# Kernel optimization log

Measured on AMD Instinct MI355X. Metric: run time of the kernel, lower is better.

## Reference

```python
import jax, jax.numpy as jnp
import numpy as np

N = 100000          # nodes
E = 3200000         # edges
C_IN = 64
HIDDEN = 64
NUM_CLASSES = 10
NUM_GRAPHS = 256
EPS = 1e-5


def _graph_conv(x, src, dst, w_rel, w_root, b):
    # PyG GraphConv(aggr='mean'): out_i = W_rel * mean_{j->i} x_j + W_root * x_i + b
    msg_sum = jax.ops.segment_sum(x[src], dst, num_segments=N)            # [N, C]
    cnt = jax.ops.segment_sum(jnp.ones((src.shape[0], 1), x.dtype), dst,
                              num_segments=N)                             # [N, 1]
    agg = msg_sum / jnp.maximum(cnt, 1.0)
    return agg @ w_rel + x @ w_root + b


def _batch_norm(x, gamma, beta):
    # PyG BatchNorm in training mode: batch stats over the node dimension
    mean = jnp.mean(x, axis=0)
    var = jnp.var(x, axis=0)
    return (x - mean) * jax.lax.rsqrt(var + EPS) * gamma + beta


def setup_inputs() -> dict:
    key = jax.random.key(0)
    ks = jax.random.split(key, 20)
    x = jax.random.normal(ks[0], (N, C_IN), dtype=jnp.float32)
    edge_index = jax.random.randint(ks[1], (2, E), 0, N, dtype=jnp.int32)
    batch = jnp.sort(jax.random.randint(ks[2], (N,), 0, NUM_GRAPHS, dtype=jnp.int32))

    def lin(k, fan_in, fan_out):
        s = 1.0 / np.sqrt(fan_in)
        return jax.random.uniform(k, (fan_in, fan_out), jnp.float32, -s, s)

    dims = [(C_IN, 16), (16, 32), (32, 32), (32, HIDDEN)]
    params = {}
    ki = 3
    for i, (ci, co) in enumerate(dims, start=1):
        params[f"w_rel{i}"] = lin(ks[ki], ci, co); ki += 1
        params[f"w_root{i}"] = lin(ks[ki], ci, co); ki += 1
        params[f"b{i}"] = jnp.zeros((co,), jnp.float32)
        params[f"g{i}"] = jnp.ones((co,), jnp.float32)
        params[f"be{i}"] = jnp.zeros((co,), jnp.float32)
    params["w_lin1"] = lin(ks[ki], HIDDEN, HIDDEN); ki += 1
    params["b_lin1"] = jnp.zeros((HIDDEN,), jnp.float32)
    params["w_lin2"] = lin(ks[ki], HIDDEN, NUM_CLASSES); ki += 1
    params["b_lin2"] = jnp.zeros((NUM_CLASSES,), jnp.float32)

    return {"x": x, "edge_index": edge_index, "batch": batch, **params}


def reference(x, edge_index, batch,
              w_rel1, w_root1, b1, g1, be1,
              w_rel2, w_root2, b2, g2, be2,
              w_rel3, w_root3, b3, g3, be3,
              w_rel4, w_root4, b4, g4, be4,
              w_lin1, b_lin1, w_lin2, b_lin2):
    src, dst = edge_index[0], edge_index[1]
    h = jax.nn.elu(_batch_norm(_graph_conv(x, src, dst, w_rel1, w_root1, b1), g1, be1))
    h = jax.nn.elu(_batch_norm(_graph_conv(h, src, dst, w_rel2, w_root2, b2), g2, be2))
    h = jax.nn.elu(_batch_norm(_graph_conv(h, src, dst, w_rel3, w_root3, b3), g3, be3))
    h = jax.nn.elu(_batch_norm(_graph_conv(h, src, dst, w_rel4, w_root4, b4), g4, be4))
    # global mean pool over graphs
    pooled = jax.ops.segment_sum(h, batch, num_segments=NUM_GRAPHS)
    cnt = jax.ops.segment_sum(jnp.ones((N, 1), h.dtype), batch, num_segments=NUM_GRAPHS)
    pooled = pooled / jnp.maximum(cnt, 1.0)
    z = jax.nn.relu(pooled @ w_lin1 + b_lin1)
    # dropout omitted (deterministic / eval mode)
    logits = z @ w_lin2 + b_lin2
    return jax.nn.log_softmax(logits, axis=-1)
```

## Files before the change

### kernel.cpp

```cpp
#include <hip/hip_runtime.h>
#include <hip/hip_bf16.h>
#include <math.h>

#define NGRAPHS 256
#define BSHIFT 8
#define NBUCK 512
#define NSORT 256
#define SBLK 256
#define SMASK 0x00FFFFFFu

__device__ __forceinline__ float bf2f(unsigned short u) {
    return __uint_as_float((unsigned)u << 16);
}
__device__ __forceinline__ unsigned short f2bf(float f) {
    unsigned u = __float_as_uint(f);
    unsigned r = (u + 0x7FFFu + ((u >> 16) & 1u)) >> 16;
    return (unsigned short)r;
}

__global__ __launch_bounds__(256) void k_bhist(const int* __restrict__ dst, int* __restrict__ hmat, int E) {
    __shared__ int hist[NBUCK];
    for (int i = threadIdx.x; i < NBUCK; i += 256) hist[i] = 0;
    __syncthreads();
    int chunk = (E + NSORT - 1) / NSORT;
    int lo = blockIdx.x * chunk;
    int hi = lo + chunk; if (hi > E) hi = E;
    for (int i = lo + threadIdx.x; i < hi; i += 256) {
        int d = __builtin_nontemporal_load(dst + i);
        atomicAdd(&hist[d >> BSHIFT], 1);
    }
    __syncthreads();
    for (int i = threadIdx.x; i < NBUCK; i += 256)
        hmat[(size_t)blockIdx.x * NBUCK + i] = hist[i];
}

__global__ __launch_bounds__(256) void k_cscan(int* __restrict__ hmat, int* __restrict__ btot) {
    int col = blockIdx.x * 256 + threadIdx.x;
    int run = 0;
#pragma unroll 4
    for (int r = 0; r < NSORT; r++) {
        int v = hmat[(size_t)r * NBUCK + col];
        hmat[(size_t)r * NBUCK + col] = run;
        run += v;
    }
    btot[col] = run;
}

__global__ __launch_bounds__(512) void k_bscan(const int* __restrict__ btot, int* __restrict__ bstart) {
    __shared__ int s[512];
    int tid = threadIdx.x;
    int v = btot[tid];
    s[tid] = v;
    __syncthreads();
    for (int off = 1; off < 512; off <<= 1) {
        int t = (tid >= off) ? s[tid - off] : 0;
        __syncthreads();
        s[tid] += t;
        __syncthreads();
    }
    bstart[tid] = s[tid] - v;
    if (tid == 511) bstart[NBUCK] = s[511];
}

__global__ __launch_bounds__(256) void k_bscatter(const int* __restrict__ src, const int* __restrict__ dst,
                                                  const int* __restrict__ hmat, const int* __restrict__ bstart,
                                                  unsigned* __restrict__ ebuf, int E) {
    __shared__ int cur[NBUCK];
    for (int i = threadIdx.x; i < NBUCK; i += 256)
        cur[i] = bstart[i] + hmat[(size_t)blockIdx.x * NBUCK + i];
    __syncthreads();
    int chunk = (E + NSORT - 1) / NSORT;
    int lo = blockIdx.x * chunk;
    int hi = lo + chunk; if (hi > E) hi = E;
    for (int i = lo + threadIdx.x; i < hi; i += 256) {
        int d = __builtin_nontemporal_load(dst + i);
        int s = __builtin_nontemporal_load(src + i);
        int p = atomicAdd(&cur[d >> BSHIFT], 1);
        ebuf[p] = (unsigned)s | ((unsigned)(d & 255) << 24);
    }
}

__global__ __launch_bounds__(256) void k_sort2(const unsigned* __restrict__ ebuf, const int* __restrict__ bstart,
                                               int* __restrict__ csr, int* __restrict__ row_start, int N) {
    __shared__ int hist[256];
    __shared__ int sc[256];
    __shared__ int scur[256];
    int b = blockIdx.x;
    int e0 = bstart[b], e1 = bstart[b + 1];
    hist[threadIdx.x] = 0;
    __syncthreads();
    for (int i = e0 + threadIdx.x; i < e1; i += 256)
        atomicAdd(&hist[__builtin_nontemporal_load(ebuf + i) >> 24], 1);
    __syncthreads();
    sc[threadIdx.x] = hist[threadIdx.x];
    __syncthreads();
    for (int off = 1; off < 256; off <<= 1) {
        int t = (threadIdx.x >= off) ? sc[threadIdx.x - off] : 0;
        __syncthreads();
        sc[threadIdx.x] += t;
        __syncthreads();
    }
    {
        int inc = sc[threadIdx.x];
        int ex = inc - hist[threadIdx.x];
        scur[threadIdx.x] = e0 + ex;
        int node = (b << BSHIFT) + threadIdx.x;
        if (node < N) row_start[node] = e0 + ex;
        if (node == N - 1) row_start[N] = e0 + inc;
    }
    __syncthreads();
    for (int i = e0 + threadIdx.x; i < e1; i += 256) {
        unsigned w = __builtin_nontemporal_load(ebuf + i);
        int p = atomicAdd(&scur[w >> 24], 1);
        csr[p] = (int)(w & SMASK);
    }
}

template <int CI, int CO, bool HAS_REL, bool HAS_ROOT, bool ADD_AGG, bool HAS_BIAS, bool IN_BF16, bool OUT_BF16>
__global__ __launch_bounds__(256) void k_lin(const void* __restrict__ hroot_v, const float* __restrict__ hrel,
                                             const float* __restrict__ w_rel, const float* __restrict__ w_root,
                                             const float* __restrict__ bias, const float* __restrict__ aggadd,
                                             float* __restrict__ out, unsigned short* __restrict__ outb, int N) {
    constexpr int QPR = CO / 4;
    __shared__ float s_rel[HAS_REL ? CI * CO : 1];
    __shared__ float s_root[HAS_ROOT ? CI * CO : 1];
    __shared__ float s_b[HAS_BIAS ? CO : 4];
    if (HAS_REL)
        for (int i = threadIdx.x; i < CI * CO; i += 256) s_rel[i] = w_rel[i];
    if (HAS_ROOT)
        for (int i = threadIdx.x; i < CI * CO; i += 256) s_root[i] = w_root[i];
    if (HAS_BIAS && threadIdx.x < CO) s_b[threadIdx.x] = bias[threadIdx.x];
    __syncthreads();

    int t = blockIdx.x * 256 + threadIdx.x;
    int n = t / QPR;
    int c0 = (t % QPR) * 4;
    if (n >= N) return;

    float rr[HAS_ROOT ? CI : 1];
    if (HAS_ROOT) {
        if (IN_BF16) {
            const ushort4* hp = (const ushort4*)((const unsigned short*)hroot_v + (size_t)n * CI);
#pragma unroll
            for (int i = 0; i < CI / 4; i++) {
                ushort4 v = hp[i];
                rr[4 * i + 0] = bf2f(v.x); rr[4 * i + 1] = bf2f(v.y);
                rr[4 * i + 2] = bf2f(v.z); rr[4 * i + 3] = bf2f(v.w);
            }
        } else {
            const float4* hp = (const float4*)((const float*)hroot_v + (size_t)n * CI);
#pragma unroll
            for (int i = 0; i < CI / 4; i++) {
                float4 v = hp[i];
                rr[4 * i + 0] = v.x; rr[4 * i + 1] = v.y; rr[4 * i + 2] = v.z; rr[4 * i + 3] = v.w;
            }
        }
    }
    float ar[HAS_REL ? CI : 1];
    if (HAS_REL) {
        const float4* mp = (const float4*)(hrel + (size_t)n * CI);
#pragma unroll
        for (int i = 0; i < CI / 4; i++) {
            float4 v = mp[i];
            ar[4 * i + 0] = v.x; ar[4 * i + 1] = v.y; ar[4 * i + 2] = v.z; ar[4 * i + 3] = v.w;
        }
    }

    float4 acc;
    if (HAS_BIAS) acc = *(const float4*)&s_b[c0];
    else { acc.x = 0.f; acc.y = 0.f; acc.z = 0.f; acc.w = 0.f; }
    if (ADD_AGG) {
        float4 v = *(const float4*)(aggadd + (size_t)n * CO + c0);
        acc.x += v.x; acc.y += v.y; acc.z += v.z; acc.w += v.w;
    }

#pragma unroll
    for (int ci = 0; ci < CI; ci++) {
        if (HAS_REL) {
            float a = ar[ci];
            float4 w = *(const float4*)&s_rel[ci * CO + c0];
            acc.x += a * w.x; acc.y += a * w.y; acc.z += a * w.z; acc.w += a * w.w;
        }
        if (HAS_ROOT) {
            float hv = rr[ci];
            float4 w = *(const float4*)&s_root[ci * CO + c0];
            acc.x += hv * w.x; acc.y += hv * w.y; acc.z += hv * w.z; acc.w += hv * w.w;
        }
    }
    if (OUT_BF16) {
        ushort4 o;
        o.x = f2bf(acc.x); o.y = f2bf(acc.y); o.z = f2bf(acc.z); o.w = f2bf(acc.w);
        *(ushort4*)(outb + (size_t)n * CO + c0) = o;
    } else {
        *(float4*)(out + (size_t)n * CO + c0) = acc;
    }
}

template <int C>
__global__ __launch_bounds__(256) void k_gather(const unsigned short* __restrict__ h,
                                                const int* __restrict__ row_start,
                                                const int* __restrict__ csr, float* __restrict__ agg, int N) {
    constexpr int LPR = C / 4;
    constexpr int EPP = 64 / LPR;
    int lane = threadIdx.x & 63;
    int wid = blockIdx.x * 4 + (threadIdx.x >> 6);
    if (wid >= N) return;
    int r0 = row_start[wid];
    int deg = row_start[wid + 1] - r0;
    int es = lane / LPR;
    int cq = (lane % LPR) * 4;
    float ax = 0.f, ay = 0.f, az = 0.f, aw = 0.f;
    for (int j0 = 0; j0 < deg; j0 += 4 * EPP) {
        int s[4]; bool p[4];
#pragma unroll
        for (int u = 0; u < 4; u++) {
            int j = j0 + u * EPP + es;
            p[u] = j < deg;
            s[u] = __builtin_nontemporal_load(&csr[r0 + (p[u] ? j : 0)]);
        }
#pragma unroll
        for (int u = 0; u < 4; u++) {
            ushort4 v = *(const ushort4*)(h + (size_t)s[u] * C + cq);
            if (p[u]) {
                ax += bf2f(v.x); ay += bf2f(v.y); az += bf2f(v.z); aw += bf2f(v.w);
            }
        }
    }
#pragma unroll
    for (int off = LPR; off < 64; off <<= 1) {
        ax += __shfl_xor(ax, off, 64);
        ay += __shfl_xor(ay, off, 64);
        az += __shfl_xor(az, off, 64);
        aw += __shfl_xor(aw, off, 64);
    }
    if (lane < LPR) {
        float rec = 1.0f / (float)(deg > 0 ? deg : 1);
        float4 o; o.x = ax * rec; o.y = ay * rec; o.z = az * rec; o.w = aw * rec;
        *(float4*)(agg + (size_t)wid * C + cq) = o;
    }
}

template <int CO>
__global__ __launch_bounds__(256) void k_stats(const float* __restrict__ h, float* __restrict__ partials, int N) {
    constexpr int QPR = CO / 4;
    int total = N * QPR;
    float s0 = 0, s1 = 0, s2 = 0, s3 = 0, q0 = 0, q1 = 0, q2 = 0, q3 = 0;
    int idx = blockIdx.x * 256 + threadIdx.x;
    for (int i = idx; i < total; i += SBLK * 256) {
        float4 v = ((const float4*)h)[i];
        s0 += v.x; q0 += v.x * v.x;
        s1 += v.y; q1 += v.y * v.y;
        s2 += v.z; q2 += v.z * v.z;
        s3 += v.w; q3 += v.w * v.w;
    }
#pragma unroll
    for (int off = QPR; off < 64; off <<= 1) {
        s0 += __shfl_xor(s0, off, 64); q0 += __shfl_xor(q0, off, 64);
        s1 += __shfl_xor(s1, off, 64); q1 += __shfl_xor(q1, off, 64);
        s2 += __shfl_xor(s2, off, 64); q2 += __shfl_xor(q2, off, 64);
        s3 += __shfl_xor(s3, off, 64); q3 += __shfl_xor(q3, off, 64);
    }
    __shared__ float part[4][2 * CO];
    int lane = threadIdx.x & 63;
    int w = threadIdx.x >> 6;
    if (lane < QPR) {
        int cq = lane * 4;
        part[w][cq + 0] = s0; part[w][CO + cq + 0] = q0;
        part[w][cq + 1] = s1; part[w][CO + cq + 1] = q1;
        part[w][cq + 2] = s2; part[w][CO + cq + 2] = q2;
        part[w][cq + 3] = s3; part[w][CO + cq + 3] = q3;
    }
    __syncthreads();
    if (threadIdx.x < 2 * CO) {
        float v = part[0][threadIdx.x] + part[1][threadIdx.x] + part[2][threadIdx.x] + part[3][threadIdx.x];
        partials[blockIdx.x * (2 * CO) + threadIdx.x] = v;
    }
}

__global__ __launch_bounds__(128) void k_sfinal(const float* __restrict__ partials, const float* __restrict__ g,
                                                const float* __restrict__ be, float* __restrict__ stats,
                                                int CO, float invN) {
    __shared__ float red[128];
    int c = threadIdx.x;
    float s = 0.f;
    if (c < 2 * CO) {
        for (int b = 0; b < SBLK; b++) s += partials[b * 2 * CO + c];
    }
    red[c] = s;
    __syncthreads();
    if (c < CO) {
        float mean = red[c] * invN;
        float var = red[CO + c] * invN - mean * mean;
        float sc = g[c] * rsqrtf(var + 1e-5f);
        stats[128 + c] = sc;
        stats[192 + c] = be[c] - mean * sc;
    }
}

template <int CO>
__global__ __launch_bounds__(256) void k_bn_elu(const float* __restrict__ h, const float* __restrict__ stats,
                                                unsigned short* __restrict__ hb, int N) {
    __shared__ float sc[CO], sh[CO];
    if (threadIdx.x < CO) {
        sc[threadIdx.x] = stats[128 + threadIdx.x];
        sh[threadIdx.x] = stats[192 + threadIdx.x];
    }
    __syncthreads();
    int total = N * (CO / 4);
    int i = blockIdx.x * 256 + threadIdx.x;
    if (i >= total) return;
    float4 v = ((const float4*)h)[i];
    int cq = (i % (CO / 4)) * 4;
    v.x = v.x * sc[cq + 0] + sh[cq + 0];
    v.y = v.y * sc[cq + 1] + sh[cq + 1];
    v.z = v.z * sc[cq + 2] + sh[cq + 2];
    v.w = v.w * sc[cq + 3] + sh[cq + 3];
    v.x = v.x > 0.f ? v.x : expm1f(v.x);
    v.y = v.y > 0.f ? v.y : expm1f(v.y);
    v.z = v.z > 0.f ? v.z : expm1f(v.z);
    v.w = v.w > 0.f ? v.w : expm1f(v.w);
    ushort4 o;
    o.x = f2bf(v.x); o.y = f2bf(v.y); o.z = f2bf(v.z); o.w = f2bf(v.w);
    ((ushort4*)hb)[i] = o;
}

__global__ __launch_bounds__(256) void k_pool(const unsigned short* __restrict__ hb, const int* __restrict__ batch,
                                              float* __restrict__ pooled, float* __restrict__ cntg, int N) {
    int lane = threadIdx.x & 63;
    int wid = blockIdx.x * 4 + (threadIdx.x >> 6);
    int n0 = wid * 64;
    if (n0 >= N) return;
    int nmax = N - n0; if (nmax > 64) nmax = 64;
    int cur = batch[n0];
    float acc = 0.f;
    int run = 0;
    for (int k = 0; k < nmax; k++) {
        int g = batch[n0 + k];
        if (g != cur) {
            atomicAdd(&pooled[(size_t)cur * 64 + lane], acc);
            if (lane == 0) atomicAdd(&cntg[cur], (float)run);
            cur = g; acc = 0.f; run = 0;
        }
        acc += bf2f(hb[(size_t)(n0 + k) * 64 + lane]);
        run++;
    }
    atomicAdd(&pooled[(size_t)cur * 64 + lane], acc);
    if (lane == 0) atomicAdd(&cntg[cur], (float)run);
}

__global__ __launch_bounds__(256) void k_head(const float* __restrict__ pooled, const float* __restrict__ cntg,
                                              const float* __restrict__ w1, const float* __restrict__ b1,
                                              const float* __restrict__ w2, const float* __restrict__ b2,
                                              float* __restrict__ out) {
    int g = threadIdx.x;
    float rec = 1.0f / fmaxf(cntg[g], 1.0f);
    float p[64];
    {
        const float4* pp = (const float4*)(pooled + (size_t)g * 64);
#pragma unroll
        for (int i = 0; i < 16; i++) {
            float4 v = pp[i];
            p[4 * i + 0] = v.x * rec; p[4 * i + 1] = v.y * rec;
            p[4 * i + 2] = v.z * rec; p[4 * i + 3] = v.w * rec;
        }
    }
    float lg[10];
#pragma unroll
    for (int t = 0; t < 10; t++) lg[t] = b2[t];
#pragma unroll 1
    for (int j = 0; j < 64; j++) {
        float a = b1[j];
#pragma unroll
        for (int k = 0; k < 64; k++) a += p[k] * w1[k * 64 + j];
        a = fmaxf(a, 0.f);
#pragma unroll
        for (int t = 0; t < 10; t++) lg[t] += a * w2[j * 10 + t];
    }
    float m = -1e30f;
#pragma unroll
    for (int t = 0; t < 10; t++) m = fmaxf(m, lg[t]);
    float s = 0.f;
#pragma unroll
    for (int t = 0; t < 10; t++) s += expf(lg[t] - m);
    float lse = m + logf(s);
#pragma unroll
    for (int t = 0; t < 10; t++) out[(size_t)g * 10 + t] = lg[t] - lse;
}

extern "C" void kernel_launch(void* const* d_in, const int* in_sizes, int n_in,
                              void* d_out, int out_size, void* d_ws, size_t ws_size,
                              hipStream_t stream) {
    const float* x = (const float*)d_in[0];
    const int* ei = (const int*)d_in[1];
    const int* batch = (const int*)d_in[2];
    const int N = in_sizes[0] / 64;
    const int E = in_sizes[1] / 2;
    const int* src = ei;
    const int* dst = ei + E;

    const float* w_rel1 = (const float*)d_in[3];
    const float* w_root1 = (const float*)d_in[4];
    const float* b1 = (const float*)d_in[5];
    const float* g1 = (const float*)d_in[6];
    const float* be1 = (const float*)d_in[7];
    const float* w_rel2 = (const float*)d_in[8];
    const float* w_root2 = (const float*)d_in[9];
    const float* b2 = (const float*)d_in[10];
    const float* g2 = (const float*)d_in[11];
    const float* be2 = (const float*)d_in[12];
    const float* w_rel3 = (const float*)d_in[13];
    const float* w_root3 = (const float*)d_in[14];
    const float* b3 = (const float*)d_in[15];
    const float* g3 = (const float*)d_in[16];
    const float* be3 = (const float*)d_in[17];
    const float* w_rel4 = (const float*)d_in[18];
    const float* w_root4 = (const float*)d_in[19];
    const float* b4 = (const float*)d_in[20];
    const float* g4 = (const float*)d_in[21];
    const float* be4 = (const float*)d_in[22];
    const float* w_lin1 = (const float*)d_in[23];
    const float* b_lin1 = (const float*)d_in[24];
    const float* w_lin2 = (const float*)d_in[25];
    const float* b_lin2 = (const float*)d_in[26];

    char* ws = (char*)d_ws;
    size_t off = 0;
    auto alloc = [&](size_t bytes) { size_t o = off; off += (bytes + 255) & ~(size_t)255; return o; };
    int* hmat = (int*)(ws + alloc((size_t)NSORT * NBUCK * 4));
    int* btot = (int*)(ws + alloc((size_t)NBUCK * 4));
    int* bstart = (int*)(ws + alloc((size_t)(NBUCK + 1) * 4));
    unsigned* ebuf = (unsigned*)(ws + alloc((size_t)E * 4));
    int* csr = (int*)(ws + alloc((size_t)E * 4));
    int* row_start = (int*)(ws + alloc((size_t)(N + 1) * 4));
    float* agg = (float*)(ws + alloc((size_t)N * 32 * 4));
    unsigned short* y1b = (unsigned short*)(ws + alloc((size_t)N * 16 * 2));
    unsigned short* hb = (unsigned short*)(ws + alloc((size_t)N * 64 * 2));
    float* bufA = (float*)(ws + alloc((size_t)N * 64 * 4));
    float* stats = (float*)(ws + alloc(4 * 256 * 4));
    float* partials = (float*)(ws + alloc((size_t)SBLK * 128 * 4));
    float* pooled = (float*)(ws + alloc((size_t)(NGRAPHS * 64 + NGRAPHS) * 4));
    float* cntg = pooled + NGRAPHS * 64;

    hipMemsetAsync(pooled, 0, (size_t)(NGRAPHS * 64 + NGRAPHS) * 4, stream);

    const float invN = 1.0f / (float)N;
    const int gbl = (N + 3) / 4;
    auto lgrid = [&](int qpr) { return (N * qpr + 255) / 256; };

    k_bhist<<<NSORT, 256, 0, stream>>>(dst, hmat, E);
    k_cscan<<<NBUCK / 256, 256, 0, stream>>>(hmat, btot);
    k_bscan<<<1, 512, 0, stream>>>(btot, bstart);
    k_bscatter<<<NSORT, 256, 0, stream>>>(src, dst, hmat, bstart, ebuf, E);
    k_sort2<<<NBUCK, 256, 0, stream>>>(ebuf, bstart, csr, row_start, N);

    k_lin<64, 16, true, false, false, false, false, true><<<lgrid(4), 256, 0, stream>>>(
        nullptr, x, w_rel1, nullptr, nullptr, nullptr, nullptr, y1b, N);
    k_gather<16><<<gbl, 256, 0, stream>>>(y1b, row_start, csr, agg, N);
    k_lin<64, 16, false, true, true, true, false, false><<<lgrid(4), 256, 0, stream>>>(
        x, nullptr, nullptr, w_root1, b1, agg, bufA, nullptr, N);
    k_stats<16><<<SBLK, 256, 0, stream>>>(bufA, partials, N);
    k_sfinal<<<1, 128, 0, stream>>>(partials, g1, be1, stats + 0, 16, invN);
    k_bn_elu<16><<<(N * 4 + 255) / 256, 256, 0, stream>>>(bufA, stats + 0, hb, N);

    k_gather<16><<<gbl, 256, 0, stream>>>(hb, row_start, csr, agg, N);
    k_lin<16, 32, true, true, false, true, true, false><<<lgrid(8), 256, 0, stream>>>(
        hb, agg, w_rel2, w_root2, b2, nullptr, bufA, nullptr, N);
    k_stats<32><<<SBLK, 256, 0, stream>>>(bufA, partials, N);
    k_sfinal<<<1, 128, 0, stream>>>(partials, g2, be2, stats + 256, 32, invN);
    k_bn_elu<32><<<(N * 8 + 255) / 256, 256, 0, stream>>>(bufA, stats + 256, hb, N);

    k_gather<32><<<gbl, 256, 0, stream>>>(hb, row_start, csr, agg, N);
    k_lin<32, 32, true, true, false, true, true, false><<<lgrid(8), 256, 0, stream>>>(
        hb, agg, w_rel3, w_root3, b3, nullptr, bufA, nullptr, N);
    k_stats<32><<<SBLK, 256, 0, stream>>>(bufA, partials, N);
    k_sfinal<<<1, 128, 0, stream>>>(partials, g3, be3, stats + 512, 32, invN);
    k_bn_elu<32><<<(N * 8 + 255) / 256, 256, 0, stream>>>(bufA, stats + 512, hb, N);

    k_gather<32><<<gbl, 256, 0, stream>>>(hb, row_start, csr, agg, N);
    k_lin<32, 64, true, true, false, true, true, false><<<lgrid(16), 256, 0, stream>>>(
        hb, agg, w_rel4, w_root4, b4, nullptr, bufA, nullptr, N);
    k_stats<64><<<SBLK, 256, 0, stream>>>(bufA, partials, N);
    k_sfinal<<<1, 128, 0, stream>>>(partials, g4, be4, stats + 768, 64, invN);
    k_bn_elu<64><<<(N * 16 + 255) / 256, 256, 0, stream>>>(bufA, stats + 768, hb, N);

    int waves = (N + 63) / 64;
    k_pool<<<(waves + 3) / 4, 256, 0, stream>>>(hb, batch, pooled, cntg, N);
    k_head<<<1, 256, 0, stream>>>(pooled, cntg, w_lin1, b_lin1, w_lin2, b_lin2, (float*)d_out);
}
```

Baseline: 625.1 us.

## Fuse neighbor gather with linear transform and fuse final BN-ELU into pooling

Replaces the separate gather kernel, the agg buffer and the following linear kernel with a single k_gconv kernel. Each wavefront aggregates a node's neighbors and then applies the rel/root weights through cross-lane shuffles. For the 32-channel layers, gathers are split into two phases by source-index half, which aims to improve cache locality. The last BN+ELU pass is folded into the pooling kernel, so the bf16 intermediate is never written. This removes agg round-trips and several launches, but the per-node matvec runs on one wavefront with global weight reads, and the phase split adds predicated extra loads.

```diff
diff --git a/kernel.cpp b/kernel.cpp
--- a/kernel.cpp
+++ b/kernel.cpp
@@ -196,12 +196,16 @@
     }
 }
 
-template <int C>
-__global__ __launch_bounds__(256) void k_gather(const unsigned short* __restrict__ h,
-                                                const int* __restrict__ row_start,
-                                                const int* __restrict__ csr, float* __restrict__ agg, int N) {
-    constexpr int LPR = C / 4;
+template <int CI, int CIR, int CO, int NPHASE, bool HAS_REL, bool ROOT_F32>
+__global__ __launch_bounds__(256) void k_gconv(const unsigned short* __restrict__ hsrc,
+                                               const void* __restrict__ hroot_v,
+                                               const int* __restrict__ row_start, const int* __restrict__ csr,
+                                               const float* __restrict__ w_rel, const float* __restrict__ w_root,
+                                               const float* __restrict__ bias,
+                                               float* __restrict__ out, int N) {
+    constexpr int LPR = CI / 4;
     constexpr int EPP = 64 / LPR;
+    constexpr int NB = 64 / EPP;
     int lane = threadIdx.x & 63;
     int wid = blockIdx.x * 4 + (threadIdx.x >> 6);
     if (wid >= N) return;
@@ -209,34 +213,86 @@
     int deg = row_start[wid + 1] - r0;
     int es = lane / LPR;
     int cq = (lane % LPR) * 4;
-    float ax = 0.f, ay = 0.f, az = 0.f, aw = 0.f;
-    for (int j0 = 0; j0 < deg; j0 += 4 * EPP) {
-        int s[4]; bool p[4];
-#pragma unroll
-        for (int u = 0; u < 4; u++) {
+    const int mid = N >> 1;
+
+    float a0 = 0.f, a1 = 0.f, a2 = 0.f, a3 = 0.f;
+    for (int j0 = 0; j0 < deg; j0 += 64) {
+        int sv[NB]; bool pj[NB];
+#pragma unroll
+        for (int u = 0; u < NB; u++) {
             int j = j0 + u * EPP + es;
-            p[u] = j < deg;
-            s[u] = __builtin_nontemporal_load(&csr[r0 + (p[u] ? j : 0)]);
-        }
-#pragma unroll
-        for (int u = 0; u < 4; u++) {
-            ushort4 v = *(const ushort4*)(h + (size_t)s[u] * C + cq);
-            if (p[u]) {
-                ax += bf2f(v.x); ay += bf2f(v.y); az += bf2f(v.z); aw += bf2f(v.w);
+            pj[u] = j < deg;
+            sv[u] = __builtin_nontemporal_load(&csr[r0 + (pj[u] ? j : 0)]);
+        }
+#pragma unroll
+        for (int ph = 0; ph < NPHASE; ph++) {
+            const int slo = (NPHASE == 1) ? 0 : (ph == 0 ? 0 : mid);
+            const int shi = (NPHASE == 1) ? N : (ph == 0 ? mid : N);
+            int s2[NB]; bool p2[NB];
+#pragma unroll
+            for (int u = 0; u < NB; u++) {
+                bool ir;
+                if constexpr (NPHASE == 1) ir = pj[u];
+                else ir = pj[u] && (sv[u] >= slo) && (sv[u] < shi);
+                p2[u] = ir;
+                s2[u] = ir ? sv[u] : slo;
             }
+            ushort4 v[NB];
+#pragma unroll
+            for (int u = 0; u < NB; u++)
+                v[u] = *(const ushort4*)(hsrc + (size_t)s2[u] * CI + cq);
+#pragma unroll
+            for (int u = 0; u < NB; u++) {
+                if (p2[u]) {
+                    a0 += bf2f(v[u].x); a1 += bf2f(v[u].y);
+                    a2 += bf2f(v[u].z); a3 += bf2f(v[u].w);
+                }
+            }
         }
     }
 #pragma unroll
     for (int off = LPR; off < 64; off <<= 1) {
-        ax += __shfl_xor(ax, off, 64);
-        ay += __shfl_xor(ay, off, 64);
-        az += __shfl_xor(az, off, 64);
-        aw += __shfl_xor(aw, off, 64);
-    }
-    if (lane < LPR) {
-        float rec = 1.0f / (float)(deg > 0 ? deg : 1);
-        float4 o; o.x = ax * rec; o.y = ay * rec; o.z = az * rec; o.w = aw * rec;
-        *(float4*)(agg + (size_t)wid * C + cq) = o;
+        a0 += __shfl_xor(a0, off, 64);
+        a1 += __shfl_xor(a1, off, 64);
+        a2 += __shfl_xor(a2, off, 64);
+        a3 += __shfl_xor(a3, off, 64);
+    }
+    float rec = 1.0f / (float)(deg > 0 ? deg : 1);
+    a0 *= rec; a1 *= rec; a2 *= rec; a3 *= rec;
+    float aa[4] = {a0, a1, a2, a3};
+
+    float rr[4];
+    if (ROOT_F32) {
+        const float4* xp = (const float4*)((const float*)hroot_v + (size_t)wid * CIR);
+        float4 v = xp[lane % (CIR / 4)];
+        rr[0] = v.x; rr[1] = v.y; rr[2] = v.z; rr[3] = v.w;
+    } else {
+        const unsigned short* hp = (const unsigned short*)hroot_v;
+        ushort4 v = *(const ushort4*)(hp + (size_t)wid * CIR + (size_t)(lane % (CIR / 4)) * 4);
+        rr[0] = bf2f(v.x); rr[1] = bf2f(v.y); rr[2] = bf2f(v.z); rr[3] = bf2f(v.w);
+    }
+
+    int c = lane;
+    if (c < CO) {
+        float acc = bias[c];
+#pragma unroll
+        for (int ci = 0; ci < CIR; ci++) {
+            float hv = __shfl(rr[ci & 3], ci >> 2, 64);
+            acc += hv * w_root[ci * CO + c];
+        }
+        if (HAS_REL) {
+#pragma unroll
+            for (int ci = 0; ci < CI; ci++) {
+                float av = __shfl(aa[ci & 3], ci >> 2, 64);
+                acc += av * w_rel[ci * CO + c];
+            }
+        } else {
+            float t0 = __shfl(a0, c >> 2, 64), t1 = __shfl(a1, c >> 2, 64);
+            float t2 = __shfl(a2, c >> 2, 64), t3 = __shfl(a3, c >> 2, 64);
+            float av = (c & 2) ? ((c & 1) ? t3 : t2) : ((c & 1) ? t1 : t0);
+            acc += av;
+        }
+        __builtin_nontemporal_store(acc, &out[(size_t)wid * CO + c]);
     }
 }
 
@@ -324,12 +380,15 @@
     ((ushort4*)hb)[i] = o;
 }
 
-__global__ __launch_bounds__(256) void k_pool(const unsigned short* __restrict__ hb, const int* __restrict__ batch,
-                                              float* __restrict__ pooled, float* __restrict__ cntg, int N) {
+__global__ __launch_bounds__(256) void k_bn_elu_pool(const float* __restrict__ h, const float* __restrict__ stats,
+                                                     const int* __restrict__ batch,
+                                                     float* __restrict__ pooled, float* __restrict__ cntg, int N) {
     int lane = threadIdx.x & 63;
     int wid = blockIdx.x * 4 + (threadIdx.x >> 6);
     int n0 = wid * 64;
     if (n0 >= N) return;
+    float scl = stats[128 + lane];
+    float shl = stats[192 + lane];
     int nmax = N - n0; if (nmax > 64) nmax = 64;
     int cur = batch[n0];
     float acc = 0.f;
@@ -341,7 +400,9 @@
             if (lane == 0) atomicAdd(&cntg[cur], (float)run);
             cur = g; acc = 0.f; run = 0;
         }
-        acc += bf2f(hb[(size_t)(n0 + k) * 64 + lane]);
+        float v = h[(size_t)(n0 + k) * 64 + lane] * scl + shl;
+        v = v > 0.f ? v : expm1f(v);
+        acc += v;
         run++;
     }
     atomicAdd(&pooled[(size_t)cur * 64 + lane], acc);
@@ -432,7 +493,6 @@
     unsigned* ebuf = (unsigned*)(ws + alloc((size_t)E * 4));
     int* csr = (int*)(ws + alloc((size_t)E * 4));
     int* row_start = (int*)(ws + alloc((size_t)(N + 1) * 4));
-    float* agg = (float*)(ws + alloc((size_t)N * 32 * 4));
     unsigned short* y1b = (unsigned short*)(ws + alloc((size_t)N * 16 * 2));
     unsigned short* hb = (unsigned short*)(ws + alloc((size_t)N * 64 * 2));
     float* bufA = (float*)(ws + alloc((size_t)N * 64 * 4));
@@ -455,35 +515,30 @@
 
     k_lin<64, 16, true, false, false, false, false, true><<<lgrid(4), 256, 0, stream>>>(
         nullptr, x, w_rel1, nullptr, nullptr, nullptr, nullptr, y1b, N);
-    k_gather<16><<<gbl, 256, 0, stream>>>(y1b, row_start, csr, agg, N);
-    k_lin<64, 16, false, true, true, true, false, false><<<lgrid(4), 256, 0, stream>>>(
-        x, nullptr, nullptr, w_root1, b1, agg, bufA, nullptr, N);
+    k_gconv<16, 64, 16, 1, false, true><<<gbl, 256, 0, stream>>>(
+        y1b, x, row_start, csr, nullptr, w_root1, b1, bufA, N);
     k_stats<16><<<SBLK, 256, 0, stream>>>(bufA, partials, N);
     k_sfinal<<<1, 128, 0, stream>>>(partials, g1, be1, stats + 0, 16, invN);
     k_bn_elu<16><<<(N * 4 + 255) / 256, 256, 0, stream>>>(bufA, stats + 0, hb, N);
 
-    k_gather<16><<<gbl, 256, 0, stream>>>(hb, row_start, csr, agg, N);
-    k_lin<16, 32, true, true, false, true, true, false><<<lgrid(8), 256, 0, stream>>>(
-        hb, agg, w_rel2, w_root2, b2, nullptr, bufA, nullptr, N);
+    k_gconv<16, 16, 32, 1, true, false><<<gbl, 256, 0, stream>>>(
+        hb, hb, row_start, csr, w_rel2, w_root2, b2, bufA, N);
     k_stats<32><<<SBLK, 256, 0, stream>>>(bufA, partials, N);
     k_sfinal<<<1, 128, 0, stream>>>(partials, g2, be2, stats + 256, 32, invN);
     k_bn_elu<32><<<(N * 8 + 255) / 256, 256, 0, stream>>>(bufA, stats + 256, hb, N);
 
-    k_gather<32><<<gbl, 256, 0, stream>>>(hb, row_start, csr, agg, N);
-    k_lin<32, 32, true, true, false, true, true, false><<<lgrid(8), 256, 0, stream>>>(
-        hb, agg, w_rel3, w_root3, b3, nullptr, bufA, nullptr, N);
+    k_gconv<32, 32, 32, 2, true, false><<<gbl, 256, 0, stream>>>(
+        hb, hb, row_start, csr, w_rel3, w_root3, b3, bufA, N);
     k_stats<32><<<SBLK, 256, 0, stream>>>(bufA, partials, N);
     k_sfinal<<<1, 128, 0, stream>>>(partials, g3, be3, stats + 512, 32, invN);
     k_bn_elu<32><<<(N * 8 + 255) / 256, 256, 0, stream>>>(bufA, stats + 512, hb, N);
 
-    k_gather<32><<<gbl, 256, 0, stream>>>(hb, row_start, csr, agg, N);
-    k_lin<32, 64, true, true, false, true, true, false><<<lgrid(16), 256, 0, stream>>>(
-        hb, agg, w_rel4, w_root4, b4, nullptr, bufA, nullptr, N);
+    k_gconv<32, 32, 64, 2, true, false><<<gbl, 256, 0, stream>>>(
+        hb, hb, row_start, csr, w_rel4, w_root4, b4, bufA, N);
     k_stats<64><<<SBLK, 256, 0, stream>>>(bufA, partials, N);
     k_sfinal<<<1, 128, 0, stream>>>(partials, g4, be4, stats + 768, 64, invN);
-    k_bn_elu<64><<<(N * 16 + 255) / 256, 256, 0, stream>>>(bufA, stats + 768, hb, N);
-
     int waves = (N + 63) / 64;
-    k_pool<<<(waves + 3) / 4, 256, 0, stream>>>(hb, batch, pooled, cntg, N);
+    k_bn_elu_pool<<<(waves + 3) / 4, 256, 0, stream>>>(bufA, stats + 768, batch, pooled, cntg, N);
+
     k_head<<<1, 256, 0, stream>>>(pooled, cntg, w_lin1, b_lin1, w_lin2, b_lin2, (float*)d_out);
 }
```

After: 763.9 us. +22.2%, slower.

## Stage CSR chunks in LDS for gather, fuse stats finalize and final BN-ELU into pooling

Applied to the files above, without the earlier changes.

The gather kernel now loads each block's contiguous CSR edge range cooperatively into shared memory and issues deeper batches of independent row loads per wave, aiming at more memory-level parallelism and fewer predicated loads. The separate BN-statistics finalize kernel is folded into k_stats through a last-block atomic counter, which removes four small launches. The last-layer BN+ELU is fused into the pooling kernel, so the bf16 activation write and reread is skipped. The cost is extra block-wide syncs in gather and an atomic counter that depends on the memset.

```diff
diff --git a/kernel.cpp b/kernel.cpp
--- a/kernel.cpp
+++ b/kernel.cpp
@@ -196,53 +196,88 @@
     }
 }
 
+#define GCHUNK 1024
 template <int C>
 __global__ __launch_bounds__(256) void k_gather(const unsigned short* __restrict__ h,
                                                 const int* __restrict__ row_start,
                                                 const int* __restrict__ csr, float* __restrict__ agg, int N) {
     constexpr int LPR = C / 4;
     constexpr int EPP = 64 / LPR;
+    constexpr int DEPTH = 32 / EPP;
+    __shared__ int sbuf[GCHUNK];
     int lane = threadIdx.x & 63;
-    int wid = blockIdx.x * 4 + (threadIdx.x >> 6);
-    if (wid >= N) return;
-    int r0 = row_start[wid];
-    int deg = row_start[wid + 1] - r0;
+    int w = threadIdx.x >> 6;
+    int nb = blockIdx.x * 4;
+    int wid = nb + w;
+    bool act = wid < N;
+    int nb_end = nb + 4; if (nb_end > N) nb_end = N;
+    int eb0 = row_start[nb];
+    int eb1 = row_start[nb_end];
+    int r0 = act ? row_start[wid] : 0;
+    int r1 = act ? row_start[wid + 1] : 0;
     int es = lane / LPR;
     int cq = (lane % LPR) * 4;
-    float ax = 0.f, ay = 0.f, az = 0.f, aw = 0.f;
-    for (int j0 = 0; j0 < deg; j0 += 4 * EPP) {
-        int s[4]; bool p[4];
-#pragma unroll
-        for (int u = 0; u < 4; u++) {
-            int j = j0 + u * EPP + es;
-            p[u] = j < deg;
-            s[u] = __builtin_nontemporal_load(&csr[r0 + (p[u] ? j : 0)]);
-        }
-#pragma unroll
-        for (int u = 0; u < 4; u++) {
-            ushort4 v = *(const ushort4*)(h + (size_t)s[u] * C + cq);
-            if (p[u]) {
-                ax += bf2f(v.x); ay += bf2f(v.y); az += bf2f(v.z); aw += bf2f(v.w);
+
+    float a0 = 0.f, a1 = 0.f, a2 = 0.f, a3 = 0.f;
+    for (int base = eb0; base < eb1; base += GCHUNK) {
+        int len = eb1 - base; if (len > GCHUNK) len = GCHUNK;
+        __syncthreads();
+        for (int i = threadIdx.x; i < len; i += 256)
+            sbuf[i] = __builtin_nontemporal_load(csr + base + i);
+        __syncthreads();
+        if (act) {
+            int lo = (r0 > base ? r0 : base) - base;
+            int hiv = r1 < base + len ? r1 : base + len;
+            int hi = hiv - base;
+            if (hi > lo) {
+                int nfull = (hi - lo) >> 5;
+                int j0 = lo;
+                for (int b = 0; b < nfull; b++, j0 += 32) {
+                    int s[DEPTH];
+#pragma unroll
+                    for (int u = 0; u < DEPTH; u++) s[u] = sbuf[j0 + u * EPP + es];
+                    ushort4 v[DEPTH];
+#pragma unroll
+                    for (int u = 0; u < DEPTH; u++)
+                        v[u] = *(const ushort4*)(h + (size_t)s[u] * C + cq);
+#pragma unroll
+                    for (int u = 0; u < DEPTH; u++) {
+                        a0 += bf2f(v[u].x); a1 += bf2f(v[u].y);
+                        a2 += bf2f(v[u].z); a3 += bf2f(v[u].w);
+                    }
+                }
+                for (int j = j0 + es; j < hi; j += EPP) {
+                    int s = sbuf[j];
+                    ushort4 v = *(const ushort4*)(h + (size_t)s * C + cq);
+                    a0 += bf2f(v.x); a1 += bf2f(v.y); a2 += bf2f(v.z); a3 += bf2f(v.w);
+                }
             }
         }
     }
 #pragma unroll
     for (int off = LPR; off < 64; off <<= 1) {
-        ax += __shfl_xor(ax, off, 64);
-        ay += __shfl_xor(ay, off, 64);
-        az += __shfl_xor(az, off, 64);
-        aw += __shfl_xor(aw, off, 64);
-    }
-    if (lane < LPR) {
+        a0 += __shfl_xor(a0, off, 64);
+        a1 += __shfl_xor(a1, off, 64);
+        a2 += __shfl_xor(a2, off, 64);
+        a3 += __shfl_xor(a3, off, 64);
+    }
+    if (act && lane < LPR) {
+        int deg = r1 - r0;
         float rec = 1.0f / (float)(deg > 0 ? deg : 1);
-        float4 o; o.x = ax * rec; o.y = ay * rec; o.z = az * rec; o.w = aw * rec;
+        float4 o; o.x = a0 * rec; o.y = a1 * rec; o.z = a2 * rec; o.w = a3 * rec;
         *(float4*)(agg + (size_t)wid * C + cq) = o;
     }
 }
 
 template <int CO>
-__global__ __launch_bounds__(256) void k_stats(const float* __restrict__ h, float* __restrict__ partials, int N) {
+__global__ __launch_bounds__(256) void k_stats(const float* __restrict__ h, float* __restrict__ partials,
+                                               const float* __restrict__ g, const float* __restrict__ be,
+                                               float* __restrict__ stats, int* __restrict__ cnt,
+                                               float invN, int N) {
     constexpr int QPR = CO / 4;
+    __shared__ float part[4][2 * CO];
+    __shared__ float red[128];
+    __shared__ int is_last;
     int total = N * QPR;
     float s0 = 0, s1 = 0, s2 = 0, s3 = 0, q0 = 0, q1 = 0, q2 = 0, q3 = 0;
     int idx = blockIdx.x * 256 + threadIdx.x;
@@ -260,7 +295,6 @@
         s2 += __shfl_xor(s2, off, 64); q2 += __shfl_xor(q2, off, 64);
         s3 += __shfl_xor(s3, off, 64); q3 += __shfl_xor(q3, off, 64);
     }
-    __shared__ float part[4][2 * CO];
     int lane = threadIdx.x & 63;
     int w = threadIdx.x >> 6;
     if (lane < QPR) {
@@ -275,18 +309,17 @@
         float v = part[0][threadIdx.x] + part[1][threadIdx.x] + part[2][threadIdx.x] + part[3][threadIdx.x];
         partials[blockIdx.x * (2 * CO) + threadIdx.x] = v;
     }
-}
-
-__global__ __launch_bounds__(128) void k_sfinal(const float* __restrict__ partials, const float* __restrict__ g,
-                                                const float* __restrict__ be, float* __restrict__ stats,
-                                                int CO, float invN) {
-    __shared__ float red[128];
+    __threadfence();
+    if (threadIdx.x == 0) is_last = (atomicAdd(cnt, 1) == SBLK - 1);
+    __syncthreads();
+    if (!is_last) return;
+    __threadfence();
     int c = threadIdx.x;
-    float s = 0.f;
     if (c < 2 * CO) {
+        float s = 0.f;
         for (int b = 0; b < SBLK; b++) s += partials[b * 2 * CO + c];
-    }
-    red[c] = s;
+        red[c] = s;
+    }
     __syncthreads();
     if (c < CO) {
         float mean = red[c] * invN;
@@ -324,28 +357,33 @@
     ((ushort4*)hb)[i] = o;
 }
 
-__global__ __launch_bounds__(256) void k_pool(const unsigned short* __restrict__ hb, const int* __restrict__ batch,
-                                              float* __restrict__ pooled, float* __restrict__ cntg, int N) {
+__global__ __launch_bounds__(256) void k_bn_elu_pool(const float* __restrict__ h, const float* __restrict__ stats,
+                                                     const int* __restrict__ batch,
+                                                     float* __restrict__ pooled, float* __restrict__ cntg, int N) {
     int lane = threadIdx.x & 63;
     int wid = blockIdx.x * 4 + (threadIdx.x >> 6);
-    int n0 = wid * 64;
+    int n0 = wid * 16;
     if (n0 >= N) return;
-    int nmax = N - n0; if (nmax > 64) nmax = 64;
+    float scl = stats[128 + lane];
+    float shl = stats[192 + lane];
+    int nmax = N - n0; if (nmax > 16) nmax = 16;
     int cur = batch[n0];
     float acc = 0.f;
-    int run = 0;
+    float run = 0.f;
     for (int k = 0; k < nmax; k++) {
         int g = batch[n0 + k];
         if (g != cur) {
             atomicAdd(&pooled[(size_t)cur * 64 + lane], acc);
-            if (lane == 0) atomicAdd(&cntg[cur], (float)run);
-            cur = g; acc = 0.f; run = 0;
-        }
-        acc += bf2f(hb[(size_t)(n0 + k) * 64 + lane]);
-        run++;
+            if (lane == 0) atomicAdd(&cntg[cur], run);
+            cur = g; acc = 0.f; run = 0.f;
+        }
+        float v = h[(size_t)(n0 + k) * 64 + lane] * scl + shl;
+        v = v > 0.f ? v : expm1f(v);
+        acc += v;
+        run += 1.f;
     }
     atomicAdd(&pooled[(size_t)cur * 64 + lane], acc);
-    if (lane == 0) atomicAdd(&cntg[cur], (float)run);
+    if (lane == 0) atomicAdd(&cntg[cur], run);
 }
 
 __global__ __launch_bounds__(256) void k_head(const float* __restrict__ pooled, const float* __restrict__ cntg,
@@ -438,10 +476,11 @@
     float* bufA = (float*)(ws + alloc((size_t)N * 64 * 4));
     float* stats = (float*)(ws + alloc(4 * 256 * 4));
     float* partials = (float*)(ws + alloc((size_t)SBLK * 128 * 4));
-    float* pooled = (float*)(ws + alloc((size_t)(NGRAPHS * 64 + NGRAPHS) * 4));
+    float* pooled = (float*)(ws + alloc((size_t)(NGRAPHS * 64 + NGRAPHS + 8) * 4));
     float* cntg = pooled + NGRAPHS * 64;
-
-    hipMemsetAsync(pooled, 0, (size_t)(NGRAPHS * 64 + NGRAPHS) * 4, stream);
+    int* cnt = (int*)(cntg + NGRAPHS);
+
+    hipMemsetAsync(pooled, 0, (size_t)(NGRAPHS * 64 + NGRAPHS + 8) * 4, stream);
 
     const float invN = 1.0f / (float)N;
     const int gbl = (N + 3) / 4;
@@ -458,32 +497,27 @@
     k_gather<16><<<gbl, 256, 0, stream>>>(y1b, row_start, csr, agg, N);
     k_lin<64, 16, false, true, true, true, false, false><<<lgrid(4), 256, 0, stream>>>(
         x, nullptr, nullptr, w_root1, b1, agg, bufA, nullptr, N);
-    k_stats<16><<<SBLK, 256, 0, stream>>>(bufA, partials, N);
-    k_sfinal<<<1, 128, 0, stream>>>(partials, g1, be1, stats + 0, 16, invN);
+    k_stats<16><<<SBLK, 256, 0, stream>>>(bufA, partials, g1, be1, stats + 0, cnt + 0, invN, N);
     k_bn_elu<16><<<(N * 4 + 255) / 256, 256, 0, stream>>>(bufA, stats + 0, hb, N);
 
     k_gather<16><<<gbl, 256, 0, stream>>>(hb, row_start, csr, agg, N);
     k_lin<16, 32, true, true, false, true, true, false><<<lgrid(8), 256, 0, stream>>>(
         hb, agg, w_rel2, w_root2, b2, nullptr, bufA, nullptr, N);
-    k_stats<32><<<SBLK, 256, 0, stream>>>(bufA, partials, N);
-    k_sfinal<<<1, 128, 0, stream>>>(partials, g2, be2, stats + 256, 32, invN);
+    k_stats<32><<<SBLK, 256, 0, stream>>>(bufA, partials, g2, be2, stats + 256, cnt + 1, invN, N);
     k_bn_elu<32><<<(N * 8 + 255) / 256, 256, 0, stream>>>(bufA, stats + 256, hb, N);
 
     k_gather<32><<<gbl, 256, 0, stream>>>(hb, row_start, csr, agg, N);
     k_lin<32, 32, true, true, false, true, true, false><<<lgrid(8), 256, 0, stream>>>(
         hb, agg, w_rel3, w_root3, b3, nullptr, bufA, nullptr, N);
-    k_stats<32><<<SBLK, 256, 0, stream>>>(bufA, partials, N);
-    k_sfinal<<<1, 128, 0, stream>>>(partials, g3, be3, stats + 512, 32, invN);
+    k_stats<32><<<SBLK, 256, 0, stream>>>(bufA, partials, g3, be3, stats + 512, cnt + 2, invN, N);
     k_bn_elu<32><<<(N * 8 + 255) / 256, 256, 0, stream>>>(bufA, stats + 512, hb, N);
 
     k_gather<32><<<gbl, 256, 0, stream>>>(hb, row_start, csr, agg, N);
     k_lin<32, 64, true, true, false, true, true, false><<<lgrid(16), 256, 0, stream>>>(
         hb, agg, w_rel4, w_root4, b4, nullptr, bufA, nullptr, N);
-    k_stats<64><<<SBLK, 256, 0, stream>>>(bufA, partials, N);
-    k_sfinal<<<1, 128, 0, stream>>>(partials, g4, be4, stats + 768, 64, invN);
-    k_bn_elu<64><<<(N * 16 + 255) / 256, 256, 0, stream>>>(bufA, stats + 768, hb, N);
-
-    int waves = (N + 63) / 64;
-    k_pool<<<(waves + 3) / 4, 256, 0, stream>>>(hb, batch, pooled, cntg, N);
+    k_stats<64><<<SBLK, 256, 0, stream>>>(bufA, partials, g4, be4, stats + 768, cnt + 3, invN, N);
+    int waves16 = (N + 15) / 16;
+    k_bn_elu_pool<<<(waves16 + 3) / 4, 256, 0, stream>>>(bufA, stats + 768, batch, pooled, cntg, N);
+
     k_head<<<1, 256, 0, stream>>>(pooled, cntg, w_lin1, b_lin1, w_lin2, b_lin2, (float*)d_out);
 }
```

Result: slower. 638.9 us (+2.2%).
